# Kernel tuning notes

Measured on AMD Instinct MI355X. Metric: run time of the kernel, lower is better.

Reference implementation:

```python
import jax, jax.numpy as jnp
import numpy as np

B, H, GRID_H, GRID_W, C = 8, 16, 64, 64, 128
R = C // 4  # N_RDIM: rotary pair dim per axis
N = GRID_H * GRID_W


def _make_cs(max_pos, r):
    # RoPE cos/sin table: [max_pos, r, 2] with cos at [...,0], sin at [...,1]
    inv_freq = 1.0 / (10000.0 ** (jnp.arange(r, dtype=jnp.float32) / r))
    ang = jnp.arange(max_pos, dtype=jnp.float32)[:, None] * inv_freq[None, :]
    return jnp.stack([jnp.cos(ang), jnp.sin(ang)], axis=-1)


def setup_inputs() -> dict:
    key = jax.random.key(0)
    kx, = jax.random.split(key, 1)
    x = jax.random.normal(kx, (B, H, N, C), dtype=jnp.float32)
    # packed indices: (row << 16) | col, as in encode_idx
    rows = jnp.arange(GRID_H, dtype=jnp.int32)
    cols = jnp.arange(GRID_W, dtype=jnp.int32)
    idx = ((rows[:, None] << 16) | cols[None, :]).reshape(-1).astype(jnp.int32)
    row_cs = _make_cs(GRID_H, R)
    col_cs = _make_cs(GRID_W, R)
    return {"x": x, "idx": idx, "row_cs": row_cs, "col_cs": col_cs}


def reference(x, idx, row_cs, col_cs):
    r = row_cs.shape[1]
    row = (idx >> 16).astype(jnp.int32)      # [N]
    col = (idx & 0xFFFF).astype(jnp.int32)   # [N]
    rc = row_cs[row]                          # [N, R, 2] gathered per token
    cc = col_cs[col]                          # [N, R, 2]
    rcos, rsin = rc[..., 0], rc[..., 1]       # [N, R]
    ccos, csin = cc[..., 0], cc[..., 1]
    x0 = x[..., 0:r]
    x1 = x[..., r:2 * r]
    x2 = x[..., 2 * r:3 * r]
    x3 = x[..., 3 * r:4 * r]
    # row rotation on first half, col rotation on second half
    y0 = x0 * rcos - x1 * rsin
    y1 = x0 * rsin + x1 * rcos
    y2 = x2 * ccos - x3 * csin
    y3 = x2 * csin + x3 * ccos
    return jnp.concatenate([y0, y1, y2, y3], axis=-1)
```

## Files before the change

kernel.cpp:

```cpp
#include <hip/hip_runtime.h>


#define NPOS 4096
#define F4_PER_ROW 32
#define BH 128
#define BH_PER_THREAD 16
#define NCHUNK (BH / BH_PER_THREAD)

__global__ __launch_bounds__(256)
void rope2d_kernel(const float4* __restrict__ x,
                   const int*    __restrict__ idx,
                   const float4* __restrict__ row_cs,
                   const float4* __restrict__ col_cs,
                   float4*       __restrict__ out)
{
    const int g = blockIdx.x * 256 + threadIdx.x;
    const int t     = g & 7;
    const int n     = (g >> 3) & (NPOS - 1);
    const int chunk = g >> 15;

    const int id   = idx[n];
    const int prow = id >> 16;
    const int pcol = id & 0xffff;

    const float4 rcs0 = row_cs[prow * 16 + t * 2];
    const float4 rcs1 = row_cs[prow * 16 + t * 2 + 1];
    const float4 ccs0 = col_cs[pcol * 16 + t * 2];
    const float4 ccs1 = col_cs[pcol * 16 + t * 2 + 1];

    long long base = ((long long)(chunk * BH_PER_THREAD) * NPOS + n) * F4_PER_ROW + t;
    const long long step = (long long)NPOS * F4_PER_ROW;

    #pragma unroll 4
    for (int i = 0; i < BH_PER_THREAD; ++i, base += step) {
        const float4 x0 = x[base];
        const float4 x1 = x[base + 8];
        const float4 x2 = x[base + 16];
        const float4 x3 = x[base + 24];

        float4 y0, y1, y2, y3;
        y0.x = x0.x * rcs0.x - x1.x * rcs0.y;   y1.x = x0.x * rcs0.y + x1.x * rcs0.x;
        y0.y = x0.y * rcs0.z - x1.y * rcs0.w;   y1.y = x0.y * rcs0.w + x1.y * rcs0.z;
        y0.z = x0.z * rcs1.x - x1.z * rcs1.y;   y1.z = x0.z * rcs1.y + x1.z * rcs1.x;
        y0.w = x0.w * rcs1.z - x1.w * rcs1.w;   y1.w = x0.w * rcs1.w + x1.w * rcs1.z;

        y2.x = x2.x * ccs0.x - x3.x * ccs0.y;   y3.x = x2.x * ccs0.y + x3.x * ccs0.x;
        y2.y = x2.y * ccs0.z - x3.y * ccs0.w;   y3.y = x2.y * ccs0.w + x3.y * ccs0.z;
        y2.z = x2.z * ccs1.x - x3.z * ccs1.y;   y3.z = x2.z * ccs1.y + x3.z * ccs1.x;
        y2.w = x2.w * ccs1.z - x3.w * ccs1.w;   y3.w = x2.w * ccs1.w + x3.w * ccs1.z;

        out[base]      = y0;
        out[base + 8]  = y1;
        out[base + 16] = y2;
        out[base + 24] = y3;
    }
}

extern "C" void kernel_launch(void* const* d_in, const int* in_sizes, int n_in,
                              void* d_out, int out_size, void* d_ws, size_t ws_size,
                              hipStream_t stream) {
    const float4* x      = (const float4*)d_in[0];
    const int*    idx    = (const int*)d_in[1];
    const float4* row_cs = (const float4*)d_in[2];
    const float4* col_cs = (const float4*)d_in[3];
    float4*       out    = (float4*)d_out;

    const int work_items = NCHUNK * NPOS * 8;
    const int block = 256;
    const int grid = work_items / block;

    rope2d_kernel<<<grid, block, 0, stream>>>(x, idx, row_cs, col_cs, out);
}
```

Measured before the change: 106.3 us.

## Use grid-stride contiguous mapping with nontemporal loads and stores

Replaces the per-thread loop over 16 batch-head slices, which strided by a full slice each iteration, with a grid-stride loop over 2048 blocks. On each iteration a wavefront now covers contiguous memory. Loads and stores of x and out use nontemporal builtins so the streaming data does not pollute cache. The trade-off is that idx and the cos/sin tables are re-read every iteration instead of being hoisted once per thread.

```diff
diff --git a/kernel.cpp b/kernel.cpp
--- a/kernel.cpp
+++ b/kernel.cpp
@@ -1,44 +1,48 @@
 #include <hip/hip_runtime.h>
 
 
+typedef float fv4 __attribute__((ext_vector_type(4)));
+
 #define NPOS 4096
 #define F4_PER_ROW 32
-#define BH 128
-#define BH_PER_THREAD 16
-#define NCHUNK (BH / BH_PER_THREAD)
+#define NBLOCK 2048
+#define NTHREAD (NBLOCK * 256)
+#define TOTAL_ITEMS (8 * 16 * NPOS * 8)
+#define ITERS (TOTAL_ITEMS / NTHREAD)
 
 __global__ __launch_bounds__(256)
-void rope2d_kernel(const float4* __restrict__ x,
-                   const int*    __restrict__ idx,
-                   const float4* __restrict__ row_cs,
-                   const float4* __restrict__ col_cs,
-                   float4*       __restrict__ out)
+void rope2d_kernel(const fv4* __restrict__ x,
+                   const int* __restrict__ idx,
+                   const fv4* __restrict__ row_cs,
+                   const fv4* __restrict__ col_cs,
+                   fv4*       __restrict__ out)
 {
-    const int g = blockIdx.x * 256 + threadIdx.x;
-    const int t     = g & 7;
-    const int n     = (g >> 3) & (NPOS - 1);
-    const int chunk = g >> 15;
+    const int tid0 = blockIdx.x * 256 + threadIdx.x;
 
-    const int id   = idx[n];
-    const int prow = id >> 16;
-    const int pcol = id & 0xffff;
+    #pragma unroll 2
+    for (int i = 0; i < ITERS; ++i) {
+        const int g     = tid0 + i * NTHREAD;
+        const int rowid = g >> 3;
+        const int t     = g & 7;
+        const int n     = rowid & (NPOS - 1);
 
-    const float4 rcs0 = row_cs[prow * 16 + t * 2];
-    const float4 rcs1 = row_cs[prow * 16 + t * 2 + 1];
-    const float4 ccs0 = col_cs[pcol * 16 + t * 2];
-    const float4 ccs1 = col_cs[pcol * 16 + t * 2 + 1];
+        const int id   = idx[n];
+        const int prow = id >> 16;
+        const int pcol = id & 0xffff;
 
-    long long base = ((long long)(chunk * BH_PER_THREAD) * NPOS + n) * F4_PER_ROW + t;
-    const long long step = (long long)NPOS * F4_PER_ROW;
+        const int base = rowid * F4_PER_ROW + t;
 
-    #pragma unroll 4
-    for (int i = 0; i < BH_PER_THREAD; ++i, base += step) {
-        const float4 x0 = x[base];
-        const float4 x1 = x[base + 8];
-        const float4 x2 = x[base + 16];
-        const float4 x3 = x[base + 24];
+        const fv4 x0 = __builtin_nontemporal_load(x + base);
+        const fv4 x1 = __builtin_nontemporal_load(x + base + 8);
+        const fv4 x2 = __builtin_nontemporal_load(x + base + 16);
+        const fv4 x3 = __builtin_nontemporal_load(x + base + 24);
 
-        float4 y0, y1, y2, y3;
+        const fv4 rcs0 = row_cs[prow * 16 + t * 2];
+        const fv4 rcs1 = row_cs[prow * 16 + t * 2 + 1];
+        const fv4 ccs0 = col_cs[pcol * 16 + t * 2];
+        const fv4 ccs1 = col_cs[pcol * 16 + t * 2 + 1];
+
+        fv4 y0, y1, y2, y3;
         y0.x = x0.x * rcs0.x - x1.x * rcs0.y;   y1.x = x0.x * rcs0.y + x1.x * rcs0.x;
         y0.y = x0.y * rcs0.z - x1.y * rcs0.w;   y1.y = x0.y * rcs0.w + x1.y * rcs0.z;
         y0.z = x0.z * rcs1.x - x1.z * rcs1.y;   y1.z = x0.z * rcs1.y + x1.z * rcs1.x;
@@ -49,25 +53,21 @@
         y2.z = x2.z * ccs1.x - x3.z * ccs1.y;   y3.z = x2.z * ccs1.y + x3.z * ccs1.x;
         y2.w = x2.w * ccs1.z - x3.w * ccs1.w;   y3.w = x2.w * ccs1.w + x3.w * ccs1.z;
 
-        out[base]      = y0;
-        out[base + 8]  = y1;
-        out[base + 16] = y2;
-        out[base + 24] = y3;
+        __builtin_nontemporal_store(y0, out + base);
+        __builtin_nontemporal_store(y1, out + base + 8);
+        __builtin_nontemporal_store(y2, out + base + 16);
+        __builtin_nontemporal_store(y3, out + base + 24);
     }
 }
 
 extern "C" void kernel_launch(void* const* d_in, const int* in_sizes, int n_in,
                               void* d_out, int out_size, void* d_ws, size_t ws_size,
                               hipStream_t stream) {
-    const float4* x      = (const float4*)d_in[0];
-    const int*    idx    = (const int*)d_in[1];
-    const float4* row_cs = (const float4*)d_in[2];
-    const float4* col_cs = (const float4*)d_in[3];
-    float4*       out    = (float4*)d_out;
+    const fv4* x      = (const fv4*)d_in[0];
+    const int* idx    = (const int*)d_in[1];
+    const fv4* row_cs = (const fv4*)d_in[2];
+    const fv4* col_cs = (const fv4*)d_in[3];
+    fv4*       out    = (fv4*)d_out;
 
-    const int work_items = NCHUNK * NPOS * 8;
-    const int block = 256;
-    const int grid = work_items / block;
-
-    rope2d_kernel<<<grid, block, 0, stream>>>(x, idx, row_cs, col_cs, out);
+    rope2d_kernel<<<NBLOCK, 256, 0, stream>>>(x, idx, row_cs, col_cs, out);
 }
```

Result: faster. 94.50 us (-11.1%).
